# Kernel optimization log

Measured on AMD Instinct MI355X. Metric: run time of the kernel, lower is better.

## Reference

```python
import jax, jax.numpy as jnp
from jax import lax
import numpy as np

NINP, NHID, T, B = 512, 1024, 512, 64


def setup_inputs() -> dict:
    key = jax.random.key(0)
    ks = jax.random.split(key, 16)
    si = 1.0 / np.sqrt(NINP)
    sh = 1.0 / np.sqrt(NHID)
    inp = {
        "input": jax.random.normal(ks[0], (T, B, NINP), dtype=jnp.float32),
        "h": jax.random.normal(ks[1], (1, B, NHID), dtype=jnp.float32),
        "Wiz_w": jax.random.uniform(ks[2], (NHID, NINP), jnp.float32, -si, si),
        "Wiz_b": jax.random.uniform(ks[3], (NHID,), jnp.float32, -si, si),
        "Wir_w": jax.random.uniform(ks[4], (NHID, NINP), jnp.float32, -si, si),
        "Wir_b": jax.random.uniform(ks[5], (NHID,), jnp.float32, -si, si),
        "Wih_w": jax.random.uniform(ks[6], (NHID, NINP), jnp.float32, -si, si),
        "Wih_b": jax.random.uniform(ks[7], (NHID,), jnp.float32, -si, si),
        "Whz_w": jax.random.uniform(ks[8], (NHID, NHID), jnp.float32, -sh, sh),
        "Whz_b": jax.random.uniform(ks[9], (NHID,), jnp.float32, -sh, sh),
        "Whr_w": jax.random.uniform(ks[10], (NHID, NHID), jnp.float32, -sh, sh),
        "Whr_b": jax.random.uniform(ks[11], (NHID,), jnp.float32, -sh, sh),
        "Whh_w": jax.random.uniform(ks[12], (NHID, NHID), jnp.float32, -sh, sh),
        "Whh_b": jax.random.uniform(ks[13], (NHID,), jnp.float32, -sh, sh),
    }
    lengths = jax.random.randint(ks[14], (B,), 1, T + 1)
    lengths = lengths.at[0].set(T)  # ensure max_length == T (static scan length)
    inp["lengths"] = lengths.astype(jnp.int64)
    return inp


def reference(input, h, Wiz_w, Wiz_b, Wir_w, Wir_b, Wih_w, Wih_b,
              Whz_w, Whz_b, Whr_w, Whr_b, Whh_w, Whh_b, lengths):
    h0 = h[0]  # squeeze(0): [B, nhid]
    # Precompute input projections for all timesteps in one batched GEMM each: [T, B, nhid]
    xz = jnp.einsum('tbi,hi->tbh', input, Wiz_w) + Wiz_b
    xr = jnp.einsum('tbi,hi->tbh', input, Wir_w) + Wir_b
    xh = jnp.einsum('tbi,hi->tbh', input, Wih_w) + Wih_b
    tsteps = jnp.arange(input.shape[0])

    def step(hprev, inputs):
        xz_t, xr_t, xh_t, t = inputs
        z = jax.nn.sigmoid(hprev @ Whz_w.T + Whz_b + xz_t)
        r = jax.nn.sigmoid(hprev @ Whr_w.T + Whr_b + xr_t)
        h_cand = jnp.tanh((r * hprev) @ Whh_w.T + Whh_b + xh_t)
        h_new = (1.0 - z) * hprev + z * h_cand
        mask = (t < lengths).astype(hprev.dtype)[:, None]  # [B, 1]
        hn = h_new * mask + hprev * (1.0 - mask)
        return hn, hn

    h_last, hidden_stacked = lax.scan(step, h0, (xz, xr, xh, tsteps))
    return hidden_stacked, h_last[None]  # ([T,B,nhid], [1,B,nhid])
```

## Files before the change

### kernel.cpp

```cpp
#include <hip/hip_runtime.h>

typedef unsigned int   uint;
typedef unsigned short ushort;

#define NINP    512
#define NHID    1024
#define T_STEPS 512
#define B_SZ    64
#define KTOT    1536
#define BN      (B_SZ * NHID)

typedef __attribute__((ext_vector_type(8))) short bf16x8;
typedef __attribute__((ext_vector_type(4))) float f32x4;
typedef __attribute__((ext_vector_type(4))) uint  uintx4;

#define WCOMB_BYTES (3 * NHID * KTOT * 2)
#define WS_BSUM     (WCOMB_BYTES)
#define WS_HP       (WS_BSUM + 3 * NHID * 4)
#define WS_RHP      (WS_HP + BN * 4)
#define WS_BAR      (WS_RHP + BN * 4)
#define WS_NEED     (WS_BAR + 16384)

#define G_SUP   256
#define G_WAKE  384

__device__ __forceinline__ float sigmoidf_(float x) { return 1.0f / (1.0f + __expf(-x)); }
__device__ __forceinline__ float tanhf_(float x)    { return 1.0f - 2.0f / (__expf(2.0f * x) + 1.0f); }

__device__ __forceinline__ ushort bf16_rne(float f) {
    uint u = __float_as_uint(f);
    return (ushort)((u + 0x7FFFu + ((u >> 16) & 1u)) >> 16);
}
__device__ __forceinline__ float bf16_to_f(ushort s) { return __uint_as_float(((uint)s) << 16); }
__device__ __forceinline__ bf16x8 ld8(const ushort* p) { return *(const bf16x8*)p; }
__device__ __forceinline__ bf16x8 cvt8(const float* p) {
    float4 a = *(const float4*)p;
    float4 b = *(const float4*)(p + 4);
    bf16x8 r;
    r[0] = (short)bf16_rne(a.x); r[1] = (short)bf16_rne(a.y);
    r[2] = (short)bf16_rne(a.z); r[3] = (short)bf16_rne(a.w);
    r[4] = (short)bf16_rne(b.x); r[5] = (short)bf16_rne(b.y);
    r[6] = (short)bf16_rne(b.z); r[7] = (short)bf16_rne(b.w);
    return r;
}
__device__ __forceinline__ f32x4 zero4() { f32x4 z = {0.f, 0.f, 0.f, 0.f}; return z; }
#define MFMA(a, b, c) __builtin_amdgcn_mfma_f32_16x16x32_bf16((a), (b), (c), 0, 0, 0)

__device__ __forceinline__ uint ld_rlx(uint* p) {
    return __hip_atomic_load(p, __ATOMIC_RELAXED, __HIP_MEMORY_SCOPE_AGENT);
}
__device__ __forceinline__ void st_rlx(uint* p, uint v) {
    __hip_atomic_store(p, v, __ATOMIC_RELAXED, __HIP_MEMORY_SCOPE_AGENT);
}
__device__ __forceinline__ uint add_rlx(uint* p, uint v) {
    return __hip_atomic_fetch_add(p, v, __ATOMIC_RELAXED, __HIP_MEMORY_SCOPE_AGENT);
}
__device__ __forceinline__ void ld_state(const uint* p, uintx4& a, uintx4& b) {
    asm volatile("global_load_dwordx4 %0, %1, off sc0 sc1"
                 : "=v"(a) : "v"(p) : "memory");
    asm volatile("global_load_dwordx4 %0, %1, off offset:16 sc0 sc1"
                 : "=v"(b) : "v"(p) : "memory");
}
__device__ __forceinline__ bf16x8 hi_frag(uintx4 a, uintx4 b) {
    uintx4 r;
    r[0] = __builtin_amdgcn_perm(a[1], a[0], 0x05040100u);
    r[1] = __builtin_amdgcn_perm(a[3], a[2], 0x05040100u);
    r[2] = __builtin_amdgcn_perm(b[1], b[0], 0x05040100u);
    r[3] = __builtin_amdgcn_perm(b[3], b[2], 0x05040100u);
    return *(bf16x8*)&r;
}
__device__ __forceinline__ bf16x8 lo_frag(uintx4 a, uintx4 b) {
    uintx4 r;
    r[0] = __builtin_amdgcn_perm(a[1], a[0], 0x07060302u);
    r[1] = __builtin_amdgcn_perm(a[3], a[2], 0x07060302u);
    r[2] = __builtin_amdgcn_perm(b[1], b[0], 0x07060302u);
    r[3] = __builtin_amdgcn_perm(b[3], b[2], 0x07060302u);
    return *(bf16x8*)&r;
}
__device__ __forceinline__ uint pack_hl(float v) {
    ushort hi = bf16_rne(v);
    ushort lo = bf16_rne(v - bf16_to_f(hi));
    return (uint)hi | ((uint)lo << 16);
}

__global__ __launch_bounds__(256) void prep_w(
    const float* __restrict__ Wiz, const float* __restrict__ Wir, const float* __restrict__ Wih,
    const float* __restrict__ Whz, const float* __restrict__ Whr, const float* __restrict__ Whh,
    ushort* __restrict__ wcomb)
{
    int tid = blockIdx.x * 256 + threadIdx.x;
    int oct = tid % (KTOT / 8);
    int row = tid / (KTOT / 8);
    int gate = row >> 10, n = row & 1023;
    int k0 = oct * 8;
    const float* src; int off;
    if (k0 < NINP) { src = gate == 0 ? Wiz : (gate == 1 ? Wir : Wih); off = n * NINP + k0; }
    else           { src = gate == 0 ? Whz : (gate == 1 ? Whr : Whh); off = n * NHID + (k0 - NINP); }
    ushort* dst = wcomb + (size_t)row * KTOT + k0;
    #pragma unroll
    for (int j = 0; j < 8; ++j) dst[j] = bf16_rne(src[off + j]);
}

__global__ __launch_bounds__(256) void prep_misc(
    const float* __restrict__ h0,
    const float* __restrict__ biz, const float* __restrict__ bir, const float* __restrict__ bih,
    const float* __restrict__ bhz, const float* __restrict__ bhr, const float* __restrict__ bhh,
    uint* __restrict__ hp, float* __restrict__ bsum, uint* __restrict__ bar)
{
    if (blockIdx.x < 256) {
        int i = blockIdx.x * 256 + threadIdx.x;
        hp[i] = pack_hl(h0[i]);
    } else {
        for (int n = threadIdx.x; n < NHID; n += 256) {
            bsum[n]            = biz[n] + bhz[n];
            bsum[NHID + n]     = bir[n] + bhr[n];
            bsum[2 * NHID + n] = bih[n] + bhh[n];
        }
        for (int i = threadIdx.x; i < 4096; i += 256) bar[i] = 0u;
    }
}

__device__ __forceinline__ void gang_arrive(uint* gbar, int oct, uint g) {
    if ((threadIdx.x & 63) == 0) {
        uint a = add_rlx(&gbar[oct * 32], 1u);
        if (a == g * 8u + 7u) {
            uint s = add_rlx(&gbar[G_SUP], 1u);
            if (s == g * 8u + 7u) {
                #pragma unroll
                for (int w = 0; w < 8; ++w) st_rlx(&gbar[G_WAKE + w * 32], g + 1u);
            }
        }
    }
}
__device__ __forceinline__ void gang_wait(uint* gbar, int oct, uint g) {
    if ((threadIdx.x & 63) == 0) {
        while (ld_rlx(&gbar[G_WAKE + oct * 32]) < g + 1u)
            __builtin_amdgcn_s_sleep(1);
    }
    asm volatile("" ::: "memory");
}

__global__ __launch_bounds__(512, 1) void gru_persist(
    const float* __restrict__ x, const float* __restrict__ h0,
    const void* __restrict__ lengths_raw,
    const ushort* __restrict__ wcomb, const float* __restrict__ bsum,
    uint* __restrict__ hp, uint* __restrict__ rhp,
    uint* __restrict__ bar, float* __restrict__ out)
{
    const int bid = blockIdx.x;
    const int nt = bid >> 2, mt = bid & 3;
    const int nbase = nt * 16, mbase = mt * 16;
    const int oct = nt >> 3;
    uint* gbar = bar + (mt << 10);
    const int tid = threadIdx.x;
    const int wv = tid >> 6, lane = tid & 63;
    const int col = lane & 15, quad = lane >> 4;
    const int q8 = quad * 8;

    __shared__ f32x4 lds_acc1[8][2][64];
    __shared__ f32x4 lds_acc2[8][64];
    __shared__ uint  lds_pad[15360];

    bf16x8 wfz[6], wfr[6], wfc[6];
    #pragma unroll
    for (int s = 0; s < 6; ++s) {
        const int j = wv + 8 * s;
        const size_t ko = (size_t)j * 32 + q8;
        wfz[s] = ld8(wcomb + (size_t)(0 * NHID + nbase + col) * KTOT + ko);
        wfr[s] = ld8(wcomb + (size_t)(1 * NHID + nbase + col) * KTOT + ko);
        wfc[s] = ld8(wcomb + (size_t)(2 * NHID + nbase + col) * KTOT + ko);
    }

    const int* l32 = (const int*)lengths_raw;
    const bool is64 = (l32[1] == 0);
    int len[4];
    float h_reg[4];
    #pragma unroll
    for (int i = 0; i < 4; ++i) {
        const int b = mbase + quad * 4 + i;
        len[i]   = is64 ? (int)((const long long*)lengths_raw)[b] : l32[b];
        h_reg[i] = h0[(size_t)b * NHID + nbase + col];
    }

    const float bias_z = bsum[nbase + col];
    const float bias_r = bsum[NHID + nbase + col];
    const float bias_c = bsum[2 * NHID + nbase + col];

    const size_t arow = (size_t)(mbase + col);

    const uint* hpp[4]; const uint* rpp[4]; size_t gi4[4];
    #pragma unroll
    for (int s = 0; s < 4; ++s) {
        const int kh = (wv + 8 * (s + 2)) * 32 - NINP;
        hpp[s] = hp  + arow * NHID + kh + q8;
        rpp[s] = rhp + arow * NHID + kh + q8;
    }
    #pragma unroll
    for (int i = 0; i < 4; ++i)
        gi4[i] = (size_t)(mbase + quad * 4 + i) * NHID + nbase + col;

    f32x4 zsig = zero4();
    bf16x8 xf[2];
    uint bgen = 0;

    f32x4 az = zero4(), ar = zero4();
    #pragma unroll
    for (int s = 0; s < 2; ++s) {
        const int k = (wv + 8 * s) * 32;
        xf[s] = cvt8(x + arow * NINP + k + q8);
        az = MFMA(xf[s], wfz[s], az);
        ar = MFMA(xf[s], wfr[s], ar);
    }

    for (int t = 0; t < T_STEPS; ++t) {
        {
            uintx4 qa[4], qb[4];
            #pragma unroll
            for (int s = 0; s < 4; ++s) ld_state(hpp[s], qa[s], qb[s]);
            asm volatile("s_waitcnt vmcnt(0)" ::: "memory");
            __builtin_amdgcn_sched_barrier(0);
            #pragma unroll
            for (int s = 0; s < 4; ++s) {
                const bf16x8 hi = hi_frag(qa[s], qb[s]);
                const bf16x8 lo = lo_frag(qa[s], qb[s]);
                az = MFMA(hi, wfz[s + 2], az);
                ar = MFMA(hi, wfr[s + 2], ar);
                az = MFMA(lo, wfz[s + 2], az);
                ar = MFMA(lo, wfr[s + 2], ar);
            }
        }
        lds_acc1[wv][0][lane] = az;
        lds_acc1[wv][1][lane] = ar;
        __syncthreads();
        if (wv == 0) {
            f32x4 rp = {bias_r, bias_r, bias_r, bias_r};
            #pragma unroll
            for (int w = 0; w < 8; ++w) {
                const f32x4 a = lds_acc1[w][1][lane];
                #pragma unroll
                for (int i = 0; i < 4; ++i) rp[i] += a[i];
            }
            #pragma unroll
            for (int i = 0; i < 4; ++i)
                st_rlx(&rhp[gi4[i]], pack_hl(sigmoidf_(rp[i]) * h_reg[i]));
            asm volatile("s_waitcnt vmcnt(0)" ::: "memory");
            gang_arrive(gbar, oct, bgen);
        }
        if (wv < 2) {
            f32x4 zp = {bias_z, bias_z, bias_z, bias_z};
            #pragma unroll
            for (int w = 0; w < 8; ++w) {
                const f32x4 a = lds_acc1[w][0][lane];
                #pragma unroll
                for (int i = 0; i < 4; ++i) zp[i] += a[i];
            }
            #pragma unroll
            for (int i = 0; i < 4; ++i) zsig[i] = sigmoidf_(zp[i]);
        }
        f32x4 ac = zero4();
        ac = MFMA(xf[0], wfc[0], ac);
        ac = MFMA(xf[1], wfc[1], ac);
        gang_wait(gbar, oct, bgen); bgen++;

        {
            uintx4 qa[4], qb[4];
            #pragma unroll
            for (int s = 0; s < 4; ++s) ld_state(rpp[s], qa[s], qb[s]);
            asm volatile("s_waitcnt vmcnt(0)" ::: "memory");
            __builtin_amdgcn_sched_barrier(0);
            #pragma unroll
            for (int s = 0; s < 4; ++s) {
                const bf16x8 hi = hi_frag(qa[s], qb[s]);
                const bf16x8 lo = lo_frag(qa[s], qb[s]);
                ac = MFMA(hi, wfc[s + 2], ac);
                ac = MFMA(lo, wfc[s + 2], ac);
            }
        }
        lds_acc2[wv][lane] = ac;
        __syncthreads();
        if (wv < 2) {
            f32x4 cp = {bias_c, bias_c, bias_c, bias_c};
            #pragma unroll
            for (int w = 0; w < 8; ++w) {
                const f32x4 a = lds_acc2[w][lane];
                #pragma unroll
                for (int i = 0; i < 4; ++i) cp[i] += a[i];
            }
            float hn4[4];
            #pragma unroll
            for (int i = 0; i < 4; ++i) {
                const float c = tanhf_(cp[i]);
                const float h = h_reg[i];
                hn4[i] = (t < len[i]) ? fmaf(zsig[i], c - h, h) : h;
                h_reg[i] = hn4[i];
            }
            if (wv == 1) {
                #pragma unroll
                for (int i = 0; i < 4; ++i) st_rlx(&hp[gi4[i]], pack_hl(hn4[i]));
                asm volatile("s_waitcnt vmcnt(0)" ::: "memory");
                gang_arrive(gbar, oct, bgen);
            } else {
                float* out_t = out + (size_t)t * BN;
                #pragma unroll
                for (int i = 0; i < 4; ++i) {
                    __builtin_nontemporal_store(hn4[i], &out_t[gi4[i]]);
                    if (t == T_STEPS - 1)
                        __builtin_nontemporal_store(hn4[i], &out[(size_t)T_STEPS * BN + gi4[i]]);
                }
            }
        }
        az = zero4(); ar = zero4();
        if (t + 1 < T_STEPS) {
            const float* x_t = x + (size_t)(t + 1) * B_SZ * NINP;
            #pragma unroll
            for (int s = 0; s < 2; ++s) {
                const int k = (wv + 8 * s) * 32;
                xf[s] = cvt8(x_t + arow * NINP + k + q8);
                az = MFMA(xf[s], wfz[s], az);
                ar = MFMA(xf[s], wfr[s], ar);
            }
        }
        gang_wait(gbar, oct, bgen); bgen++;
    }

    if (blockIdx.x == 0xFFFFFFFFu) {
        lds_pad[threadIdx.x] = bgen;
        out[0] = (float)lds_pad[threadIdx.x];
    }
}

__global__ void gru_ws_probe_mb(float* p) {
    if (blockIdx.x == 0xFFFFFFFFu) p[0] = 0.f;
}

extern "C" void kernel_launch(void* const* d_in, const int* in_sizes, int n_in,
                              void* d_out, int out_size, void* d_ws, size_t ws_size,
                              hipStream_t stream) {
    const float* x   = (const float*)d_in[0];
    const float* h0  = (const float*)d_in[1];
    const float* Wiz = (const float*)d_in[2];  const float* biz = (const float*)d_in[3];
    const float* Wir = (const float*)d_in[4];  const float* bir = (const float*)d_in[5];
    const float* Wih = (const float*)d_in[6];  const float* bih = (const float*)d_in[7];
    const float* Whz = (const float*)d_in[8];  const float* bhz = (const float*)d_in[9];
    const float* Whr = (const float*)d_in[10]; const float* bhr = (const float*)d_in[11];
    const float* Whh = (const float*)d_in[12]; const float* bhh = (const float*)d_in[13];
    const void*  lengths = d_in[14];
    float* out = (float*)d_out;
    char*  ws  = (char*)d_ws;

    size_t mb = ws_size >> 20; if (mb > 2048) mb = 2048;
    gru_ws_probe_mb<<<dim3((uint)mb + 1), 64, 0, stream>>>((float*)d_ws);
    if (ws_size < (size_t)WS_NEED) return;

    ushort* wcomb = (ushort*)ws;
    float*  bsum  = (float*)(ws + WS_BSUM);
    uint*   hp    = (uint*)(ws + WS_HP);
    uint*   rhp   = (uint*)(ws + WS_RHP);
    uint*   bar   = (uint*)(ws + WS_BAR);

    prep_w<<<2304, 256, 0, stream>>>(Wiz, Wir, Wih, Whz, Whr, Whh, wcomb);
    prep_misc<<<257, 256, 0, stream>>>(h0, biz, bir, bih, bhz, bhr, bhh, hp, bsum, bar);
    gru_persist<<<256, 512, 0, stream>>>(x, h0, lengths, wcomb, bsum,
                                         hp, rhp, bar, out);
}
```

Measured before the change: 4.762 ms.

## Replace hierarchical gang barriers with per-producer flag polling dataflow sync

Removes the two-level atomic counter barrier (octet counters plus supervisor and wake words) used twice per timestep. Each block now publishes per-step flags for its r*h and h outputs, and each wave polls only the eight producer blocks whose K-slices it consumes, spreading the polls across lanes with a wave-wide __all. This drops the global all-to-all barrier in favour of point-to-point dependencies, and lets fast blocks run ahead. The LDS accumulator is double-buffered by step parity so the tighter coupling does not overwrite data still being read. The cost is more polling traffic and a larger flag region in the workspace.

```diff
diff --git a/kernel.cpp b/kernel.cpp
--- a/kernel.cpp
+++ b/kernel.cpp
@@ -19,10 +19,9 @@
 #define WS_HP       (WS_BSUM + 3 * NHID * 4)
 #define WS_RHP      (WS_HP + BN * 4)
 #define WS_BAR      (WS_RHP + BN * 4)
-#define WS_NEED     (WS_BAR + 16384)
-
-#define G_SUP   256
-#define G_WAKE  384
+#define WS_NEED     (WS_BAR + 65536)
+
+#define FH_OFF  8192
 
 __device__ __forceinline__ float sigmoidf_(float x) { return 1.0f / (1.0f + __expf(-x)); }
 __device__ __forceinline__ float tanhf_(float x)    { return 1.0f - 2.0f / (__expf(2.0f * x) + 1.0f); }
@@ -52,14 +51,21 @@
 __device__ __forceinline__ void st_rlx(uint* p, uint v) {
     __hip_atomic_store(p, v, __ATOMIC_RELAXED, __HIP_MEMORY_SCOPE_AGENT);
 }
-__device__ __forceinline__ uint add_rlx(uint* p, uint v) {
-    return __hip_atomic_fetch_add(p, v, __ATOMIC_RELAXED, __HIP_MEMORY_SCOPE_AGENT);
-}
 __device__ __forceinline__ void ld_state(const uint* p, uintx4& a, uintx4& b) {
     asm volatile("global_load_dwordx4 %0, %1, off sc0 sc1"
                  : "=v"(a) : "v"(p) : "memory");
     asm volatile("global_load_dwordx4 %0, %1, off offset:16 sc0 sc1"
                  : "=v"(b) : "v"(p) : "memory");
+}
+__device__ __forceinline__ void poll_ge(const uint* p, uint target) {
+    for (;;) {
+        uint v;
+        asm volatile("global_load_dword %0, %1, off sc0 sc1\n\t"
+                     "s_waitcnt vmcnt(0)"
+                     : "=v"(v) : "v"(p) : "memory");
+        if (__all(v >= target)) break;
+        __builtin_amdgcn_s_sleep(1);
+    }
 }
 __device__ __forceinline__ bf16x8 hi_frag(uintx4 a, uintx4 b) {
     uintx4 r;
@@ -116,28 +122,8 @@
             bsum[NHID + n]     = bir[n] + bhr[n];
             bsum[2 * NHID + n] = bih[n] + bhh[n];
         }
-        for (int i = threadIdx.x; i < 4096; i += 256) bar[i] = 0u;
-    }
-}
-
-__device__ __forceinline__ void gang_arrive(uint* gbar, int oct, uint g) {
-    if ((threadIdx.x & 63) == 0) {
-        uint a = add_rlx(&gbar[oct * 32], 1u);
-        if (a == g * 8u + 7u) {
-            uint s = add_rlx(&gbar[G_SUP], 1u);
-            if (s == g * 8u + 7u) {
-                #pragma unroll
-                for (int w = 0; w < 8; ++w) st_rlx(&gbar[G_WAKE + w * 32], g + 1u);
-            }
-        }
-    }
-}
-__device__ __forceinline__ void gang_wait(uint* gbar, int oct, uint g) {
-    if ((threadIdx.x & 63) == 0) {
-        while (ld_rlx(&gbar[G_WAKE + oct * 32]) < g + 1u)
-            __builtin_amdgcn_s_sleep(1);
-    }
-    asm volatile("" ::: "memory");
+        for (int i = threadIdx.x; i < 16384; i += 256) bar[i] = 0u;
+    }
 }
 
 __global__ __launch_bounds__(512, 1) void gru_persist(
@@ -150,16 +136,22 @@
     const int bid = blockIdx.x;
     const int nt = bid >> 2, mt = bid & 3;
     const int nbase = nt * 16, mbase = mt * 16;
-    const int oct = nt >> 3;
-    uint* gbar = bar + (mt << 10);
     const int tid = threadIdx.x;
     const int wv = tid >> 6, lane = tid & 63;
     const int col = lane & 15, quad = lane >> 4;
     const int q8 = quad * 8;
 
-    __shared__ f32x4 lds_acc1[8][2][64];
+    __shared__ f32x4 lds_acc1[2][8][2][64];
     __shared__ f32x4 lds_acc2[8][64];
-    __shared__ uint  lds_pad[15360];
+    __shared__ uint  lds_pad[11264];
+    lds_pad[tid & 1023] = tid;
+
+    const int pslot = lane & 7;
+    const int prod  = 2 * wv + 16 * (pslot >> 1) + (pslot & 1);
+    uint* fr_ptr = bar + ((size_t)(mt * 64 + prod)) * 32;
+    uint* fh_ptr = bar + FH_OFF + ((size_t)(mt * 64 + prod)) * 32;
+    uint* my_fr  = bar + ((size_t)(mt * 64 + nt)) * 32;
+    uint* my_fh  = bar + FH_OFF + ((size_t)(mt * 64 + nt)) * 32;
 
     bf16x8 wfz[6], wfr[6], wfc[6];
     #pragma unroll
@@ -201,7 +193,6 @@
 
     f32x4 zsig = zero4();
     bf16x8 xf[2];
-    uint bgen = 0;
 
     f32x4 az = zero4(), ar = zero4();
     #pragma unroll
@@ -213,6 +204,8 @@
     }
 
     for (int t = 0; t < T_STEPS; ++t) {
+        const int par = t & 1;
+        if (t) poll_ge(fh_ptr, (uint)t);
         {
             uintx4 qa[4], qb[4];
             #pragma unroll
@@ -229,14 +222,14 @@
                 ar = MFMA(lo, wfr[s + 2], ar);
             }
         }
-        lds_acc1[wv][0][lane] = az;
-        lds_acc1[wv][1][lane] = ar;
+        lds_acc1[par][wv][0][lane] = az;
+        lds_acc1[par][wv][1][lane] = ar;
         __syncthreads();
         if (wv == 0) {
             f32x4 rp = {bias_r, bias_r, bias_r, bias_r};
             #pragma unroll
             for (int w = 0; w < 8; ++w) {
-                const f32x4 a = lds_acc1[w][1][lane];
+                const f32x4 a = lds_acc1[par][w][1][lane];
                 #pragma unroll
                 for (int i = 0; i < 4; ++i) rp[i] += a[i];
             }
@@ -244,13 +237,13 @@
             for (int i = 0; i < 4; ++i)
                 st_rlx(&rhp[gi4[i]], pack_hl(sigmoidf_(rp[i]) * h_reg[i]));
             asm volatile("s_waitcnt vmcnt(0)" ::: "memory");
-            gang_arrive(gbar, oct, bgen);
+            if (lane == 0) st_rlx(my_fr, (uint)(t + 1));
         }
         if (wv < 2) {
             f32x4 zp = {bias_z, bias_z, bias_z, bias_z};
             #pragma unroll
             for (int w = 0; w < 8; ++w) {
-                const f32x4 a = lds_acc1[w][0][lane];
+                const f32x4 a = lds_acc1[par][w][0][lane];
                 #pragma unroll
                 for (int i = 0; i < 4; ++i) zp[i] += a[i];
             }
@@ -260,8 +253,8 @@
         f32x4 ac = zero4();
         ac = MFMA(xf[0], wfc[0], ac);
         ac = MFMA(xf[1], wfc[1], ac);
-        gang_wait(gbar, oct, bgen); bgen++;
-
+
+        poll_ge(fr_ptr, (uint)(t + 1));
         {
             uintx4 qa[4], qb[4];
             #pragma unroll
@@ -298,7 +291,7 @@
                 #pragma unroll
                 for (int i = 0; i < 4; ++i) st_rlx(&hp[gi4[i]], pack_hl(hn4[i]));
                 asm volatile("s_waitcnt vmcnt(0)" ::: "memory");
-                gang_arrive(gbar, oct, bgen);
+                if (lane == 0) st_rlx(my_fh, (uint)(t + 1));
             } else {
                 float* out_t = out + (size_t)t * BN;
                 #pragma unroll
@@ -320,13 +313,10 @@
                 ar = MFMA(xf[s], wfr[s], ar);
             }
         }
-        gang_wait(gbar, oct, bgen); bgen++;
-    }
-
-    if (blockIdx.x == 0xFFFFFFFFu) {
-        lds_pad[threadIdx.x] = bgen;
-        out[0] = (float)lds_pad[threadIdx.x];
-    }
+    }
+
+    if (ld_rlx(&bar[1023]) == 0xDEADBEEFu)
+        out[0] = (float)lds_pad[tid & 1023];
 }
 
 __global__ void gru_ws_probe_mb(float* p) {
```

After: 4.141 ms. -13.0%, faster.
